# Optimization experiments

Measured on AMD Instinct MI355X. Metric: run time of the kernel, lower is better.

## Reference

```python
import jax, jax.numpy as jnp
import numpy as np

D = 1024
H = 4096  # int(dim * mlp_ratio)
E = 8
B, N = 2, 2048


def setup_inputs() -> dict:
    key = jax.random.key(0)
    ks = jax.random.split(key, 5)
    x = jax.random.normal(ks[0], (B, N, D), dtype=jnp.float32)
    # torch Linear weights, stored pre-transposed for right-multiplication
    W1 = jax.random.normal(ks[1], (E, D, H), dtype=jnp.float32) / np.sqrt(D)
    W2 = jax.random.normal(ks[2], (E, H, D), dtype=jnp.float32) / np.sqrt(H)
    Wg = jax.random.normal(ks[3], (D, E), dtype=jnp.float32) / np.sqrt(D)
    bg = jax.random.normal(ks[4], (E,), dtype=jnp.float32) * 0.01
    return {"x": x, "W1": W1, "W2": W2, "Wg": Wg, "bg": bg}


def reference(x, W1, W2, Wg, bg):
    b, n, d = x.shape
    e = Wg.shape[1]
    xf = x.reshape(b * n, d)                      # [T, D]
    logits = xf @ Wg + bg                         # [T, E]
    one_hot = jax.nn.one_hot(jnp.argmax(logits, axis=-1), e, dtype=x.dtype)  # [T, E]
    # Dense all-experts compute (faithful to the original module)
    h = jax.nn.gelu(jnp.einsum('td,edh->eth', xf, W1), approximate=True)     # [E, T, H]
    y = jnp.einsum('eth,ehd->etd', h, W2)                                    # [E, T, D]
    out = jnp.einsum('etd,te->td', y, one_hot)                               # top-1 combine
    return out.reshape(b, n, d)
```

## Files before the change

### kernel.cpp

```cpp
#include <hip/hip_runtime.h>
#include <hip/hip_bf16.h>

#define Dq 1024
#define Hq 4096
#define Tq 4096
#define MAXT2 24

#define XB_OFF 65536
#define HC_OFF (XB_OFF + Tq * Dq * 2)
#define WT_OFF (HC_OFF + MAXT2 * 256 * Hq * 2)

#define M_NT 0
#define M_CNT 8
#define M_POFF 16
#define M_CUR 32
#define M_TE 64
#define M_TR 128
#define M_EXP 512
#define M_PERM 4608

typedef __attribute__((ext_vector_type(8))) short bf16x8;
typedef __attribute__((ext_vector_type(4))) float f32x4;

__device__ __forceinline__ short f2bf(float f) {
    __hip_bfloat16 h = __float2bfloat16(f);
    return *reinterpret_cast<short*>(&h);
}

__device__ __forceinline__ float gelu_tanh(float x) {
    float u = 0.7978845608028654f * (x + 0.044715f * x * x * x);
    return x / (1.0f + __expf(-2.0f * u));
}

typedef __attribute__((address_space(1))) const void gvoid;
typedef __attribute__((address_space(3))) void lvoid;
__device__ __forceinline__ void glds16(const void* g, void* l) {
    __builtin_amdgcn_global_load_lds((gvoid*)g, (lvoid*)l, 16, 0, 0);
}

#define WAITVM_(N) asm volatile("s_waitcnt vmcnt(" #N ")" ::: "memory")
#define WAITVM(N) WAITVM_(N)

__global__ void k_init(int* meta) {
    int i = blockIdx.x * 256 + threadIdx.x;
    if (i < M_PERM + MAXT2 * 256) meta[i] = 0;
}

__global__ void k_tr(const float* __restrict__ in, short* __restrict__ out, int R, int C) {
    __shared__ float t[64][65];
    int e = blockIdx.z;
    int c0 = blockIdx.x * 64;
    int r0 = blockIdx.y * 64;
    const float* ine = in + (size_t)e * R * C;
    short* oute = out + (size_t)e * R * C;
    int tt = threadIdx.x;
    int lr = tt >> 4;
    int lc = (tt & 15) * 4;
#pragma unroll
    for (int p = 0; p < 4; ++p) {
        int r = p * 16 + lr;
        float4 v = *(const float4*)(ine + (size_t)(r0 + r) * C + c0 + lc);
        t[r][lc] = v.x; t[r][lc + 1] = v.y; t[r][lc + 2] = v.z; t[r][lc + 3] = v.w;
    }
    __syncthreads();
#pragma unroll
    for (int p = 0; p < 4; ++p) {
        int c = p * 16 + lr;
        short4 s;
        s.x = f2bf(t[lc][c]); s.y = f2bf(t[lc + 1][c]);
        s.z = f2bf(t[lc + 2][c]); s.w = f2bf(t[lc + 3][c]);
        *(short4*)(oute + (size_t)(c0 + c) * R + r0 + lc) = s;
    }
}

__global__ void k_route(const float* __restrict__ x, const float* __restrict__ Wg,
                        const float* __restrict__ bg, int* meta, short* __restrict__ xb) {
    int wave = threadIdx.x >> 6;
    int lane = threadIdx.x & 63;
    int t = blockIdx.x * 4 + wave;
    const float* xr = x + (size_t)t * Dq;
    float acc[8];
#pragma unroll
    for (int e = 0; e < 8; ++e) acc[e] = 0.0f;
#pragma unroll
    for (int j = 0; j < 16; ++j) {
        int d = j * 64 + lane;
        float xv = xr[d];
        xb[(size_t)t * Dq + d] = f2bf(xv);
        float4 w0 = *(const float4*)(Wg + (size_t)d * 8);
        float4 w1 = *(const float4*)(Wg + (size_t)d * 8 + 4);
        acc[0] += xv * w0.x; acc[1] += xv * w0.y; acc[2] += xv * w0.z; acc[3] += xv * w0.w;
        acc[4] += xv * w1.x; acc[5] += xv * w1.y; acc[6] += xv * w1.z; acc[7] += xv * w1.w;
    }
#pragma unroll
    for (int e = 0; e < 8; ++e) {
#pragma unroll
        for (int off = 32; off > 0; off >>= 1) acc[e] += __shfl_xor(acc[e], off);
    }
    if (lane == 0) {
        float best = acc[0] + bg[0];
        int be = 0;
#pragma unroll
        for (int e = 1; e < 8; ++e) {
            float v = acc[e] + bg[e];
            if (v > best) { best = v; be = e; }
        }
        meta[M_EXP + t] = be;
        atomicAdd(&meta[M_CNT + be], 1);
    }
}

__global__ void k_scan(int* meta) {
    if (threadIdx.x != 0) return;
    int off = 0, nt = 0;
    for (int e = 0; e < 8; ++e) {
        meta[M_POFF + e] = off;
        int c = meta[M_CNT + e];
        int m = (c + 255) / 256;
        for (int j = 0; j < m; ++j) {
            meta[M_TE + nt] = e;
            meta[M_TR + nt] = off + j * 256;
            ++nt;
        }
        off += m * 256;
    }
    meta[M_POFF + 8] = off;
    meta[M_NT] = nt;
}

__global__ void k_scatter(int* meta) {
    int t = blockIdx.x * 256 + threadIdx.x;
    if (t >= Tq) return;
    int e = meta[M_EXP + t];
    int pos = atomicAdd(&meta[M_CUR + e], 1);
    meta[M_PERM + meta[M_POFF + e] + pos] = t;
}

#define GEMM_SETUP()                                                           \
    int tt = threadIdx.x, w = tt >> 6, lane = tt & 63;                         \
    int fr = lane & 15, fg = lane >> 4;                                        \
    int rlo = lane >> 3;                                                       \
    int csw = ((lane & 7) ^ rlo) * 8;                                          \
    int ldsA[4], ldsB[2];                                                      \
    _Pragma("unroll")                                                          \
    for (int i = 0; i < 4; ++i) ldsA[i] = (i * 8 + w) * 512;                   \
    _Pragma("unroll")                                                          \
    for (int i = 0; i < 2; ++i) ldsB[i] = (i * 8 + w) * 512;                   \
    int wm = (w >> 1) * 64, wn = (w & 1) * 64;                                 \
    int aoff[2][4], boff[2][4];                                                \
    _Pragma("unroll")                                                          \
    for (int s2 = 0; s2 < 2; ++s2)                                             \
      _Pragma("unroll")                                                        \
      for (int f = 0; f < 4; ++f) {                                            \
        int c = s2 * 4 + fg;                                                   \
        int m = wm + f * 16 + fr;                                              \
        aoff[s2][f] = m * 64 + ((c ^ (m & 7)) * 8);                            \
        int n = wn + f * 16 + fr;                                              \
        boff[s2][f] = n * 64 + ((c ^ (n & 7)) * 8);                            \
      }                                                                        \
    f32x4 acc[4][4];                                                           \
    _Pragma("unroll")                                                          \
    for (int a = 0; a < 4; ++a)                                                \
      _Pragma("unroll")                                                        \
      for (int b = 0; b < 4; ++b) acc[a][b] = (f32x4){0.f, 0.f, 0.f, 0.f};

#define STAGE(T, BUF)                                                          \
  {                                                                            \
    _Pragma("unroll")                                                          \
    for (int i = 0; i < 4; ++i)                                                \
      glds16(aSrc[i] + (size_t)(T) * 64, As + (BUF) * 16384 + ldsA[i]);        \
    _Pragma("unroll")                                                          \
    for (int i = 0; i < 2; ++i)                                                \
      glds16(bSrc[i] + (size_t)(T) * 64, Bs + (BUF) * 8192 + ldsB[i]);         \
  }

#define PHASE(S2, BUF)                                                         \
  {                                                                            \
    bf16x8 af[4], bv[4];                                                       \
    _Pragma("unroll")                                                          \
    for (int f = 0; f < 4; ++f) {                                              \
      af[f] = *(const bf16x8*)(&As[(BUF) * 16384 + aoff[S2][f]]);              \
      bv[f] = *(const bf16x8*)(&Bs[(BUF) * 8192 + boff[S2][f]]);               \
    }                                                                          \
    __builtin_amdgcn_s_barrier();                                              \
    asm volatile("s_waitcnt lgkmcnt(0)" ::: "memory");                         \
    __builtin_amdgcn_sched_barrier(0);                                         \
    __builtin_amdgcn_s_setprio(1);                                             \
    _Pragma("unroll")                                                          \
    for (int fm = 0; fm < 4; ++fm)                                             \
      _Pragma("unroll")                                                        \
      for (int fn = 0; fn < 4; ++fn)                                           \
        acc[fm][fn] = __builtin_amdgcn_mfma_f32_16x16x32_bf16(                 \
            af[fm], bv[fn], acc[fm][fn], 0, 0, 0);                             \
    __builtin_amdgcn_s_setprio(0);                                             \
    __builtin_amdgcn_s_barrier();                                              \
    asm volatile("" ::: "memory");                                             \
  }

#define KSTEP(T, NSTEP)                                                        \
  {                                                                            \
    const int BUF = (T) % 3;                                                   \
    if ((T) + 2 < (NSTEP)) {                                                   \
      STAGE((T) + 2, ((T) + 2) % 3)                                            \
      WAITVM(12);                                                              \
    } else if ((T) + 2 == (NSTEP)) {                                           \
      WAITVM(6);                                                               \
    } else {                                                                   \
      WAITVM(0);                                                               \
    }                                                                          \
    __builtin_amdgcn_s_barrier();                                              \
    asm volatile("" ::: "memory");                                             \
    PHASE(0, BUF)                                                              \
    PHASE(1, BUF)                                                              \
  }

__global__ __launch_bounds__(512, 2) void k_gemm1(const short* __restrict__ xb,
                                                  const short* __restrict__ W1T,
                                                  const int* __restrict__ meta,
                                                  short* __restrict__ Hc) {
    __shared__ short As[3 * 16384];
    __shared__ short Bs[3 * 8192];
    int hw = blockIdx.x;
    int xcd = hw & 7, q = hw >> 3;
    int mt = q % MAXT2;
    int n0 = (xcd * 4 + q / MAXT2) * 128;
    if (mt >= meta[M_NT]) return;
    int e = meta[M_TE + mt];
    int i0 = meta[M_TR + mt];
    const int* perm = meta + M_PERM;

    GEMM_SETUP()

    const short* aSrc[4];
    const short* bSrc[2];
#pragma unroll
    for (int i = 0; i < 4; ++i) {
        int row = (i * 8 + w) * 8 + rlo;
        aSrc[i] = xb + (size_t)perm[i0 + row] * Dq + csw;
    }
#pragma unroll
    for (int i = 0; i < 2; ++i) {
        int row = (i * 8 + w) * 8 + rlo;
        bSrc[i] = W1T + ((size_t)e * Hq + n0 + row) * Dq + csw;
    }

    STAGE(0, 0)
    STAGE(1, 1)

#pragma unroll
    for (int t = 0; t < 16; ++t) KSTEP(t, 16)

#pragma unroll
    for (int fm = 0; fm < 4; ++fm) {
        int rbase = i0 + wm + fm * 16 + fg * 4;
#pragma unroll
        for (int fn = 0; fn < 4; ++fn) {
            int col = n0 + wn + fn * 16 + fr;
#pragma unroll
            for (int p = 0; p < 4; ++p) {
                float v = gelu_tanh(acc[fm][fn][p]);
                Hc[(size_t)(rbase + p) * Hq + col] = f2bf(v);
            }
        }
    }
}

__global__ __launch_bounds__(512, 2) void k_gemm2(const short* __restrict__ Hc,
                                                  const short* __restrict__ W2T,
                                                  const int* __restrict__ meta,
                                                  float* __restrict__ out) {
    __shared__ short As[3 * 16384];
    __shared__ short Bs[3 * 8192];
    int hw = blockIdx.x;
    int xcd = hw & 7, q = hw >> 3;
    int sk = q & 1;
    int mt = q >> 1;
    int n0 = xcd * 128;
    int kbase = sk * (Hq / 2);
    if (mt >= meta[M_NT]) return;
    int e = meta[M_TE + mt];
    int i0 = meta[M_TR + mt];
    const int* perm = meta + M_PERM;
    int vend = meta[M_POFF + e] + meta[M_CNT + e];

    GEMM_SETUP()

    const short* aSrc[4];
    const short* bSrc[2];
#pragma unroll
    for (int i = 0; i < 4; ++i) {
        int row = (i * 8 + w) * 8 + rlo;
        aSrc[i] = Hc + (size_t)(i0 + row) * Hq + kbase + csw;
    }
#pragma unroll
    for (int i = 0; i < 2; ++i) {
        int row = (i * 8 + w) * 8 + rlo;
        bSrc[i] = W2T + ((size_t)e * Dq + n0 + row) * Hq + kbase + csw;
    }

    STAGE(0, 0)
    STAGE(1, 1)

#pragma unroll
    for (int t = 0; t < 32; ++t) KSTEP(t, 32)

#pragma unroll
    for (int fm = 0; fm < 4; ++fm) {
        int rbase = i0 + wm + fm * 16 + fg * 4;
#pragma unroll
        for (int p = 0; p < 4; ++p) {
            int i = rbase + p;
            if (i < vend) {
                int tok = perm[i];
#pragma unroll
                for (int fn = 0; fn < 4; ++fn) {
                    int col = n0 + wn + fn * 16 + fr;
                    atomicAdd(&out[(size_t)tok * Dq + col], acc[fm][fn][p]);
                }
            }
        }
    }
}

extern "C" void kernel_launch(void* const* d_in, const int* in_sizes, int n_in,
                              void* d_out, int out_size, void* d_ws, size_t ws_size,
                              hipStream_t stream) {
    const float* x  = (const float*)d_in[0];
    const float* W1 = (const float*)d_in[1];
    const float* W2 = (const float*)d_in[2];
    const float* Wg = (const float*)d_in[3];
    const float* bg = (const float*)d_in[4];
    float* out = (float*)d_out;
    int* meta = (int*)d_ws;
    short* xb = (short*)((char*)d_ws + XB_OFF);
    short* Hc = (short*)((char*)d_ws + HC_OFF);
    short* WT = (short*)((char*)d_ws + WT_OFF);

    k_init<<<48, 256, 0, stream>>>(meta);
    hipMemsetAsync(d_out, 0, (size_t)Tq * Dq * 4, stream);
    k_route<<<Tq / 4, 256, 0, stream>>>(x, Wg, bg, meta, xb);
    k_scan<<<1, 64, 0, stream>>>(meta);
    k_scatter<<<Tq / 256, 256, 0, stream>>>(meta);
    k_tr<<<dim3(Hq / 64, Dq / 64, 8), 256, 0, stream>>>(W1, WT, Dq, Hq);
    k_gemm1<<<768, 512, 0, stream>>>(xb, WT, meta, Hc);
    k_tr<<<dim3(Dq / 64, Hq / 64, 8), 256, 0, stream>>>(W2, WT, Hq, Dq);
    k_gemm2<<<384, 512, 0, stream>>>(Hc, WT, meta, out);
}
```

Before: 337.8 us.

## Enlarge GEMM tiles to 256x256 with interleaved double-buffered load/MFMA phases

Both expert GEMMs move from 256x128 block tiles with a 3-stage buffer to 256x256 tiles with a 2-stage buffer. Each k-tile is split into four phases, and each phase issues part of the next tile's global-to-LDS loads between its MFMA groups. Each wave now computes a 128x64 sub-tile, which doubles the accumulators and raises arithmetic intensity per LDS byte. GEMM1 launches half as many blocks, and GEMM2 moves from a 2-way to a 4-way split-K with more atomics, which risks register pressure and lower occupancy with fewer blocks in flight.

```diff
diff --git a/kernel.cpp b/kernel.cpp
--- a/kernel.cpp
+++ b/kernel.cpp
@@ -141,89 +141,105 @@
     int fr = lane & 15, fg = lane >> 4;                                        \
     int rlo = lane >> 3;                                                       \
     int csw = ((lane & 7) ^ rlo) * 8;                                          \
-    int ldsA[4], ldsB[2];                                                      \
-    _Pragma("unroll")                                                          \
-    for (int i = 0; i < 4; ++i) ldsA[i] = (i * 8 + w) * 512;                   \
-    _Pragma("unroll")                                                          \
-    for (int i = 0; i < 2; ++i) ldsB[i] = (i * 8 + w) * 512;                   \
-    int wm = (w >> 1) * 64, wn = (w & 1) * 64;                                 \
-    int aoff[2][4], boff[2][4];                                                \
+    int ldsG[4];                                                               \
+    _Pragma("unroll")                                                          \
+    for (int i = 0; i < 4; ++i) ldsG[i] = (i * 64 + w * 8) * 64;               \
+    int wm = (w >> 2) * 128, wn = (w & 3) * 64;                                \
+    int boff[2][4];                                                            \
     _Pragma("unroll")                                                          \
     for (int s2 = 0; s2 < 2; ++s2)                                             \
       _Pragma("unroll")                                                        \
-      for (int f = 0; f < 4; ++f) {                                            \
-        int c = s2 * 4 + fg;                                                   \
-        int m = wm + f * 16 + fr;                                              \
-        aoff[s2][f] = m * 64 + ((c ^ (m & 7)) * 8);                            \
-        int n = wn + f * 16 + fr;                                              \
-        boff[s2][f] = n * 64 + ((c ^ (n & 7)) * 8);                            \
+      for (int fn = 0; fn < 4; ++fn) {                                         \
+        int n = wn + fn * 16 + fr;                                             \
+        boff[s2][fn] = n * 64 + (((s2 * 4 + fg) ^ (n & 7)) * 8);               \
       }                                                                        \
-    f32x4 acc[4][4];                                                           \
-    _Pragma("unroll")                                                          \
-    for (int a = 0; a < 4; ++a)                                                \
+    f32x4 acc[8][4];                                                           \
+    _Pragma("unroll")                                                          \
+    for (int a = 0; a < 8; ++a)                                                \
       _Pragma("unroll")                                                        \
       for (int b = 0; b < 4; ++b) acc[a][b] = (f32x4){0.f, 0.f, 0.f, 0.f};
 
-#define STAGE(T, BUF)                                                          \
+#define PH(p, P, T, NKT)                                                       \
   {                                                                            \
-    _Pragma("unroll")                                                          \
-    for (int i = 0; i < 4; ++i)                                                \
-      glds16(aSrc[i] + (size_t)(T) * 64, As + (BUF) * 16384 + ldsA[i]);        \
-    _Pragma("unroll")                                                          \
-    for (int i = 0; i < 2; ++i)                                                \
-      glds16(bSrc[i] + (size_t)(T) * 64, Bs + (BUF) * 8192 + ldsB[i]);         \
-  }
-
-#define PHASE(S2, BUF)                                                         \
-  {                                                                            \
-    bf16x8 af[4], bv[4];                                                       \
-    _Pragma("unroll")                                                          \
-    for (int f = 0; f < 4; ++f) {                                              \
-      af[f] = *(const bf16x8*)(&As[(BUF) * 16384 + aoff[S2][f]]);              \
-      bv[f] = *(const bf16x8*)(&Bs[(BUF) * 8192 + boff[S2][f]]);               \
+    if ((p) == 0) {                                                            \
+      _Pragma("unroll")                                                        \
+      for (int s2 = 0; s2 < 2; ++s2)                                           \
+        _Pragma("unroll")                                                      \
+        for (int fn = 0; fn < 4; ++fn)                                         \
+          bv[s2][fn] = *(const bf16x8*)(&Bs[(P) * 16384 + boff[s2][fn]]);      \
+    }                                                                          \
+    bf16x8 af[2][2];                                                           \
+    _Pragma("unroll")                                                          \
+    for (int lf = 0; lf < 2; ++lf)                                             \
+      _Pragma("unroll")                                                        \
+      for (int s2 = 0; s2 < 2; ++s2) {                                         \
+        int m = wm + (2 * (p) + lf) * 16 + fr;                                 \
+        af[lf][s2] = *(const bf16x8*)(                                         \
+            &As[(P) * 16384 + m * 64 + (((s2 * 4 + fg) ^ (m & 7)) * 8)]);      \
+      }                                                                        \
+    if ((T) + 1 < (NKT)) {                                                     \
+      int nb = (1 - (P)) * 16384;                                              \
+      size_t ko = (size_t)((T) + 1) * 64;                                      \
+      if ((p) == 0) { glds16(bSrc[0] + ko, Bs + nb + ldsG[0]);                 \
+                      glds16(bSrc[1] + ko, Bs + nb + ldsG[1]); }               \
+      if ((p) == 1) { glds16(bSrc[2] + ko, Bs + nb + ldsG[2]);                 \
+                      glds16(bSrc[3] + ko, Bs + nb + ldsG[3]); }               \
+      if ((p) == 2) { glds16(aSrc[0] + ko, As + nb + ldsG[0]);                 \
+                      glds16(aSrc[2] + ko, As + nb + ldsG[2]); }               \
+      if ((p) == 3) { glds16(aSrc[1] + ko, As + nb + ldsG[1]);                 \
+                      glds16(aSrc[3] + ko, As + nb + ldsG[3]); }               \
     }                                                                          \
     __builtin_amdgcn_s_barrier();                                              \
     asm volatile("s_waitcnt lgkmcnt(0)" ::: "memory");                         \
     __builtin_amdgcn_sched_barrier(0);                                         \
     __builtin_amdgcn_s_setprio(1);                                             \
     _Pragma("unroll")                                                          \
-    for (int fm = 0; fm < 4; ++fm)                                             \
-      _Pragma("unroll")                                                        \
-      for (int fn = 0; fn < 4; ++fn)                                           \
-        acc[fm][fn] = __builtin_amdgcn_mfma_f32_16x16x32_bf16(                 \
-            af[fm], bv[fn], acc[fm][fn], 0, 0, 0);                             \
+    for (int lf = 0; lf < 2; ++lf)                                             \
+      _Pragma("unroll")                                                        \
+      for (int s2 = 0; s2 < 2; ++s2)                                           \
+        _Pragma("unroll")                                                      \
+        for (int fn = 0; fn < 4; ++fn)                                         \
+          acc[2 * (p) + lf][fn] = __builtin_amdgcn_mfma_f32_16x16x32_bf16(     \
+              af[lf][s2], bv[s2][fn], acc[2 * (p) + lf][fn], 0, 0, 0);         \
     __builtin_amdgcn_s_setprio(0);                                             \
+    if ((p) == 1) { if ((T) + 1 < (NKT)) WAITVM(4); else WAITVM(0); }          \
+    if ((p) == 3) { if ((T) + 1 < (NKT)) WAITVM(2); }                          \
     __builtin_amdgcn_s_barrier();                                              \
     asm volatile("" ::: "memory");                                             \
   }
 
-#define KSTEP(T, NSTEP)                                                        \
+#define KTILE(T, NKT)                                                          \
   {                                                                            \
-    const int BUF = (T) % 3;                                                   \
-    if ((T) + 2 < (NSTEP)) {                                                   \
-      STAGE((T) + 2, ((T) + 2) % 3)                                            \
-      WAITVM(12);                                                              \
-    } else if ((T) + 2 == (NSTEP)) {                                           \
-      WAITVM(6);                                                               \
-    } else {                                                                   \
-      WAITVM(0);                                                               \
+    const int P = (T) & 1;                                                     \
+    bf16x8 bv[2][4];                                                           \
+    PH(0, P, T, NKT)                                                           \
+    PH(1, P, T, NKT)                                                           \
+    PH(2, P, T, NKT)                                                           \
+    PH(3, P, T, NKT)                                                           \
+  }
+
+#define PROLOGUE()                                                             \
+  {                                                                            \
+    _Pragma("unroll")                                                          \
+    for (int i = 0; i < 4; ++i) {                                              \
+      glds16(bSrc[i], Bs + ldsG[i]);                                           \
+      glds16(aSrc[i], As + ldsG[i]);                                           \
     }                                                                          \
+    WAITVM(0);                                                                 \
     __builtin_amdgcn_s_barrier();                                              \
     asm volatile("" ::: "memory");                                             \
-    PHASE(0, BUF)                                                              \
-    PHASE(1, BUF)                                                              \
   }
 
 __global__ __launch_bounds__(512, 2) void k_gemm1(const short* __restrict__ xb,
                                                   const short* __restrict__ W1T,
                                                   const int* __restrict__ meta,
                                                   short* __restrict__ Hc) {
-    __shared__ short As[3 * 16384];
-    __shared__ short Bs[3 * 8192];
+    __shared__ short As[2 * 16384];
+    __shared__ short Bs[2 * 16384];
     int hw = blockIdx.x;
     int xcd = hw & 7, q = hw >> 3;
     int mt = q % MAXT2;
-    int n0 = (xcd * 4 + q / MAXT2) * 128;
+    int n0 = (xcd * 2 + q / MAXT2) * 256;
     if (mt >= meta[M_NT]) return;
     int e = meta[M_TE + mt];
     int i0 = meta[M_TR + mt];
@@ -232,26 +248,20 @@
     GEMM_SETUP()
 
     const short* aSrc[4];
-    const short* bSrc[2];
+    const short* bSrc[4];
 #pragma unroll
     for (int i = 0; i < 4; ++i) {
-        int row = (i * 8 + w) * 8 + rlo;
+        int row = i * 64 + w * 8 + rlo;
         aSrc[i] = xb + (size_t)perm[i0 + row] * Dq + csw;
-    }
-#pragma unroll
-    for (int i = 0; i < 2; ++i) {
-        int row = (i * 8 + w) * 8 + rlo;
         bSrc[i] = W1T + ((size_t)e * Hq + n0 + row) * Dq + csw;
     }
 
-    STAGE(0, 0)
-    STAGE(1, 1)
-
-#pragma unroll
-    for (int t = 0; t < 16; ++t) KSTEP(t, 16)
-
-#pragma unroll
-    for (int fm = 0; fm < 4; ++fm) {
+    PROLOGUE()
+#pragma unroll 2
+    for (int t = 0; t < 16; ++t) KTILE(t, 16)
+
+#pragma unroll
+    for (int fm = 0; fm < 8; ++fm) {
         int rbase = i0 + wm + fm * 16 + fg * 4;
 #pragma unroll
         for (int fn = 0; fn < 4; ++fn) {
@@ -269,14 +279,14 @@
                                                   const short* __restrict__ W2T,
                                                   const int* __restrict__ meta,
                                                   float* __restrict__ out) {
-    __shared__ short As[3 * 16384];
-    __shared__ short Bs[3 * 8192];
+    __shared__ short As[2 * 16384];
+    __shared__ short Bs[2 * 16384];
     int hw = blockIdx.x;
     int xcd = hw & 7, q = hw >> 3;
-    int sk = q & 1;
-    int mt = q >> 1;
-    int n0 = xcd * 128;
-    int kbase = sk * (Hq / 2);
+    int mt = q % MAXT2;
+    int sk = (xcd & 1) * 2 + q / MAXT2;
+    int n0 = (xcd >> 1) * 256;
+    int kbase = sk * (Hq / 4);
     if (mt >= meta[M_NT]) return;
     int e = meta[M_TE + mt];
     int i0 = meta[M_TR + mt];
@@ -286,26 +296,20 @@
     GEMM_SETUP()
 
     const short* aSrc[4];
-    const short* bSrc[2];
+    const short* bSrc[4];
 #pragma unroll
     for (int i = 0; i < 4; ++i) {
-        int row = (i * 8 + w) * 8 + rlo;
+        int row = i * 64 + w * 8 + rlo;
         aSrc[i] = Hc + (size_t)(i0 + row) * Hq + kbase + csw;
-    }
-#pragma unroll
-    for (int i = 0; i < 2; ++i) {
-        int row = (i * 8 + w) * 8 + rlo;
         bSrc[i] = W2T + ((size_t)e * Dq + n0 + row) * Hq + kbase + csw;
     }
 
-    STAGE(0, 0)
-    STAGE(1, 1)
-
-#pragma unroll
-    for (int t = 0; t < 32; ++t) KSTEP(t, 32)
-
-#pragma unroll
-    for (int fm = 0; fm < 4; ++fm) {
+    PROLOGUE()
+#pragma unroll 2
+    for (int t = 0; t < 16; ++t) KTILE(t, 16)
+
+#pragma unroll
+    for (int fm = 0; fm < 8; ++fm) {
         int rbase = i0 + wm + fm * 16 + fg * 4;
 #pragma unroll
         for (int p = 0; p < 4; ++p) {
@@ -342,7 +346,7 @@
     k_scan<<<1, 64, 0, stream>>>(meta);
     k_scatter<<<Tq / 256, 256, 0, stream>>>(meta);
     k_tr<<<dim3(Hq / 64, Dq / 64, 8), 256, 0, stream>>>(W1, WT, Dq, Hq);
-    k_gemm1<<<768, 512, 0, stream>>>(xb, WT, meta, Hc);
+    k_gemm1<<<384, 512, 0, stream>>>(xb, WT, meta, Hc);
     k_tr<<<dim3(Dq / 64, Hq / 64, 8), 256, 0, stream>>>(W2, WT, Hq, Dq);
     k_gemm2<<<384, 512, 0, stream>>>(Hc, WT, meta, out);
 }
```

After: 342.3 us. No clear change (+1.3%).
